# Kernel tuning notes

Measured on AMD Instinct MI355X. Metric: run time of the kernel, lower is better.

The kernel has to match this reference:

```python
import jax, jax.numpy as jnp
import numpy as np

CROP_H, CROP_W = 14, 14
EXTRAP = 0.0


def setup_inputs() -> dict:
    key = jax.random.key(0)
    k1, k2, k3 = jax.random.split(key, 3)
    image = jax.random.normal(k1, (8, 256, 200, 200), dtype=jnp.float32)
    boxes = jax.random.uniform(k2, (512, 4), dtype=jnp.float32)  # normalized [y1,x1,y2,x2]
    box_indices = jax.random.randint(k3, (512,), 0, 8).astype(jnp.int32)
    return {"image": image, "boxes": boxes, "box_indices": box_indices}


def _crop_and_resize(image, boxes, box_indices, crop_h, crop_w, extrap):
    # TF-style crop_and_resize with bilinear sampling (matches crop_and_resize_cpu).
    B, C, H, W = image.shape
    N = boxes.shape[0]
    y1, x1, y2, x2 = boxes[:, 0], boxes[:, 1], boxes[:, 2], boxes[:, 3]
    h_scale = (y2 - y1) * (H - 1) / (crop_h - 1)
    w_scale = (x2 - x1) * (W - 1) / (crop_w - 1)
    in_y = y1[:, None] * (H - 1) + jnp.arange(crop_h, dtype=jnp.float32)[None, :] * h_scale[:, None]  # [N,ch]
    in_x = x1[:, None] * (W - 1) + jnp.arange(crop_w, dtype=jnp.float32)[None, :] * w_scale[:, None]  # [N,cw]
    valid_y = (in_y >= 0) & (in_y <= H - 1)  # [N,ch]
    valid_x = (in_x >= 0) & (in_x <= W - 1)  # [N,cw]

    y_floor = jnp.floor(in_y)
    x_floor = jnp.floor(in_x)
    ly = (in_y - y_floor)[:, :, None, None]  # [N,ch,1,1]
    lx = (in_x - x_floor)[:, None, :, None]  # [N,1,cw,1]
    y0 = jnp.clip(y_floor, 0, H - 1).astype(jnp.int32)
    y1i = jnp.clip(jnp.ceil(in_y), 0, H - 1).astype(jnp.int32)
    x0 = jnp.clip(x_floor, 0, W - 1).astype(jnp.int32)
    x1i = jnp.clip(jnp.ceil(in_x), 0, W - 1).astype(jnp.int32)

    b = box_indices.astype(jnp.int32)[:, None, None]  # [N,1,1]

    def gather(yi, xi):
        # advanced indices [N,ch,cw] separated by ':' slice -> result [N,ch,cw,C]
        return image[b, :, yi[:, :, None], xi[:, None, :]]

    tl = gather(y0, x0)
    tr = gather(y0, x1i)
    bl = gather(y1i, x0)
    br = gather(y1i, x1i)

    top = tl + (tr - tl) * lx
    bot = bl + (br - bl) * lx
    val = top + (bot - top) * ly  # [N,ch,cw,C]

    mask = (valid_y[:, :, None] & valid_x[:, None, :])[:, :, :, None]
    val = jnp.where(mask, val, jnp.float32(extrap))
    return jnp.transpose(val, (0, 3, 1, 2))  # [N,C,ch,cw]


def reference(image, boxes, box_indices):
    return _crop_and_resize(image, boxes, box_indices, CROP_H, CROP_W, EXTRAP)
```

## Files before the change

### kernel.cpp

```cpp
#include <hip/hip_runtime.h>

#define CROP_H 14
#define CROP_W 14
#define NBOX   512
#define CH     256
#define IMH    200
#define IMW    200
#define PER_BOX (CH * CROP_H * CROP_W)
#define BLOCKS_PER_BOX (PER_BOX / 256)

__global__ __launch_bounds__(256) void CropAndResize_60146722013533_kernel(
    const float* __restrict__ image,
    const float* __restrict__ boxes,
    const int*   __restrict__ box_idx,
    float*       __restrict__ out)
{
    const int n = blockIdx.x;
    const int t = threadIdx.x;

    __shared__ int   sy0[CROP_H], sy1[CROP_H], sx0[CROP_W], sx1[CROP_W];
    __shared__ float sly[CROP_H], slx[CROP_W];
    __shared__ int   svy[CROP_H], svx[CROP_W];
    __shared__ int   sb;

    if (t < CROP_H + CROP_W) {
        const float by1 = boxes[n * 4 + 0];
        const float bx1 = boxes[n * 4 + 1];
        const float by2 = boxes[n * 4 + 2];
        const float bx2 = boxes[n * 4 + 3];
        if (t < CROP_H) {
            const int gy = t;
            float h_scale = (by2 - by1) * (float)(IMH - 1) / (float)(CROP_H - 1);
            float in_y = by1 * (float)(IMH - 1) + (float)gy * h_scale;
            svy[gy] = (in_y >= 0.0f && in_y <= (float)(IMH - 1)) ? 1 : 0;
            float yf = floorf(in_y);
            sly[gy] = in_y - yf;
            sy0[gy] = (int)fminf(fmaxf(yf, 0.0f), (float)(IMH - 1));
            sy1[gy] = (int)fminf(fmaxf(ceilf(in_y), 0.0f), (float)(IMH - 1));
        } else {
            const int gx = t - CROP_H;
            float w_scale = (bx2 - bx1) * (float)(IMW - 1) / (float)(CROP_W - 1);
            float in_x = bx1 * (float)(IMW - 1) + (float)gx * w_scale;
            svx[gx] = (in_x >= 0.0f && in_x <= (float)(IMW - 1)) ? 1 : 0;
            float xf = floorf(in_x);
            slx[gx] = in_x - xf;
            sx0[gx] = (int)fminf(fmaxf(xf, 0.0f), (float)(IMW - 1));
            sx1[gx] = (int)fminf(fmaxf(ceilf(in_x), 0.0f), (float)(IMW - 1));
        }
    }
    if (t == 0) sb = box_idx[n];
    __syncthreads();

    const int elem = blockIdx.y * 256 + t;
    const int c  = elem / (CROP_H * CROP_W);
    const int r  = elem - c * (CROP_H * CROP_W);
    const int gy = r / CROP_W;
    const int gx = r - gy * CROP_W;

    const float* base = image + ((size_t)(sb * CH + c)) * (size_t)(IMH * IMW);
    const int y0  = sy0[gy];
    const int y1i = sy1[gy];
    const int x0  = sx0[gx];
    const int x1i = sx1[gx];
    const float ly = sly[gy];
    const float lx = slx[gx];

    const int xb = (x0 < IMW - 2) ? x0 : (IMW - 2);
    const float* rowt = base + y0  * IMW + xb;
    const float* rowb = base + y1i * IMW + xb;
    float2 vt, vb;
    __builtin_memcpy(&vt, rowt, 8);
    __builtin_memcpy(&vb, rowb, 8);

    const float tl = (x0  == xb) ? vt.x : vt.y;
    const float tr = (x1i == xb) ? vt.x : vt.y;
    const float bl = (x0  == xb) ? vb.x : vb.y;
    const float br = (x1i == xb) ? vb.x : vb.y;

    const float top = tl + (tr - tl) * lx;
    const float bot = bl + (br - bl) * lx;
    float val = top + (bot - top) * ly;
    if (!(svy[gy] & svx[gx])) val = 0.0f;

    out[(size_t)n * PER_BOX + elem] = val;
}

extern "C" void kernel_launch(void* const* d_in, const int* in_sizes, int n_in,
                              void* d_out, int out_size, void* d_ws, size_t ws_size,
                              hipStream_t stream) {
    const float* image   = (const float*)d_in[0];
    const float* boxes   = (const float*)d_in[1];
    const int*   box_idx = (const int*)d_in[2];
    float* out = (float*)d_out;

    dim3 grid(NBOX, BLOCKS_PER_BOX, 1);
    dim3 block(256, 1, 1);
    CropAndResize_60146722013533_kernel<<<grid, block, 0, stream>>>(image, boxes, box_idx, out);
}
```

Measured before the change: 493.0 us.

## Map threads to crop positions and loop over channel groups per block

Each block now covers one box and a group of 32 channels. Each thread owns one of the 196 crop positions, computes its sampling coordinates once in registers, and loops over channels, so the shared-memory setup and barrier are gone. Output writes use nontemporal stores. In exchange there are far fewer blocks, 60 of every 256 threads sit idle, and each thread runs a serial loop of dependent loads, which may reduce memory-level parallelism.

After: 530.5 us. +7.6%, slower.

```diff
diff --git a/kernel.cpp b/kernel.cpp
--- a/kernel.cpp
+++ b/kernel.cpp
@@ -6,83 +6,80 @@
 #define CH     256
 #define IMH    200
 #define IMW    200
-#define PER_BOX (CH * CROP_H * CROP_W)
-#define BLOCKS_PER_BOX (PER_BOX / 256)
+#define PLANE   (IMH * IMW)
+#define NPOS    (CROP_H * CROP_W)
+#define PER_BOX (CH * NPOS)
+#define CGROUPS 8
+#define CPG     (CH / CGROUPS)
 
-__global__ __launch_bounds__(256) void CropAndResize_60146722013533_kernel(
+__global__ __launch_bounds__(256, 8) void CropAndResize_60146722013533_kernel(
     const float* __restrict__ image,
     const float* __restrict__ boxes,
     const int*   __restrict__ box_idx,
     float*       __restrict__ out)
 {
-    const int n = blockIdx.x;
-    const int t = threadIdx.x;
+    const int n  = blockIdx.x;
+    const int cg = blockIdx.y;
+    const int t  = threadIdx.x;
+    if (t >= NPOS) return;
 
-    __shared__ int   sy0[CROP_H], sy1[CROP_H], sx0[CROP_W], sx1[CROP_W];
-    __shared__ float sly[CROP_H], slx[CROP_W];
-    __shared__ int   svy[CROP_H], svx[CROP_W];
-    __shared__ int   sb;
+    const int gy = t / CROP_W;
+    const int gx = t - gy * CROP_W;
 
-    if (t < CROP_H + CROP_W) {
-        const float by1 = boxes[n * 4 + 0];
-        const float bx1 = boxes[n * 4 + 1];
-        const float by2 = boxes[n * 4 + 2];
-        const float bx2 = boxes[n * 4 + 3];
-        if (t < CROP_H) {
-            const int gy = t;
-            float h_scale = (by2 - by1) * (float)(IMH - 1) / (float)(CROP_H - 1);
-            float in_y = by1 * (float)(IMH - 1) + (float)gy * h_scale;
-            svy[gy] = (in_y >= 0.0f && in_y <= (float)(IMH - 1)) ? 1 : 0;
-            float yf = floorf(in_y);
-            sly[gy] = in_y - yf;
-            sy0[gy] = (int)fminf(fmaxf(yf, 0.0f), (float)(IMH - 1));
-            sy1[gy] = (int)fminf(fmaxf(ceilf(in_y), 0.0f), (float)(IMH - 1));
-        } else {
-            const int gx = t - CROP_H;
-            float w_scale = (bx2 - bx1) * (float)(IMW - 1) / (float)(CROP_W - 1);
-            float in_x = bx1 * (float)(IMW - 1) + (float)gx * w_scale;
-            svx[gx] = (in_x >= 0.0f && in_x <= (float)(IMW - 1)) ? 1 : 0;
-            float xf = floorf(in_x);
-            slx[gx] = in_x - xf;
-            sx0[gx] = (int)fminf(fmaxf(xf, 0.0f), (float)(IMW - 1));
-            sx1[gx] = (int)fminf(fmaxf(ceilf(in_x), 0.0f), (float)(IMW - 1));
-        }
+    const float by1 = boxes[n * 4 + 0];
+    const float bx1 = boxes[n * 4 + 1];
+    const float by2 = boxes[n * 4 + 2];
+    const float bx2 = boxes[n * 4 + 3];
+    const int   b   = box_idx[n];
+
+    const float h_scale = (by2 - by1) * (float)(IMH - 1) / (float)(CROP_H - 1);
+    const float w_scale = (bx2 - bx1) * (float)(IMW - 1) / (float)(CROP_W - 1);
+    const float in_y = by1 * (float)(IMH - 1) + (float)gy * h_scale;
+    const float in_x = bx1 * (float)(IMW - 1) + (float)gx * w_scale;
+
+    const bool valid = (in_y >= 0.0f) && (in_y <= (float)(IMH - 1)) &&
+                       (in_x >= 0.0f) && (in_x <= (float)(IMW - 1));
+
+    const float yf = floorf(in_y);
+    const float xf = floorf(in_x);
+    const float ly = in_y - yf;
+    const float lx = in_x - xf;
+
+    const int y0  = (int)fminf(fmaxf(yf,          0.0f), (float)(IMH - 1));
+    const int y1i = (int)fminf(fmaxf(ceilf(in_y), 0.0f), (float)(IMH - 1));
+    const int x0  = (int)fminf(fmaxf(xf,          0.0f), (float)(IMW - 1));
+    const int x1i = (int)fminf(fmaxf(ceilf(in_x), 0.0f), (float)(IMW - 1));
+
+    const int  xb    = (x0 < IMW - 2) ? x0 : (IMW - 2);
+    const int  offt  = y0  * IMW + xb;
+    const int  offb  = y1i * IMW + xb;
+    const bool selt0 = (x0  == xb);
+    const bool selt1 = (x1i == xb);
+
+    const float* plane = image + (size_t)(b * CH + cg * CPG) * (size_t)PLANE;
+    float*       o     = out + (size_t)n * PER_BOX + (size_t)(cg * CPG) * NPOS + t;
+
+    #pragma unroll 4
+    for (int c = 0; c < CPG; ++c) {
+        float2 vt, vb;
+        __builtin_memcpy(&vt, plane + offt, 8);
+        __builtin_memcpy(&vb, plane + offb, 8);
+
+        const float tl = selt0 ? vt.x : vt.y;
+        const float tr = selt1 ? vt.x : vt.y;
+        const float bl = selt0 ? vb.x : vb.y;
+        const float br = selt1 ? vb.x : vb.y;
+
+        const float top = tl + (tr - tl) * lx;
+        const float bot = bl + (br - bl) * lx;
+        float val = top + (bot - top) * ly;
+        if (!valid) val = 0.0f;
+
+        __builtin_nontemporal_store(val, o);
+
+        plane += PLANE;
+        o     += NPOS;
     }
-    if (t == 0) sb = box_idx[n];
-    __syncthreads();
-
-    const int elem = blockIdx.y * 256 + t;
-    const int c  = elem / (CROP_H * CROP_W);
-    const int r  = elem - c * (CROP_H * CROP_W);
-    const int gy = r / CROP_W;
-    const int gx = r - gy * CROP_W;
-
-    const float* base = image + ((size_t)(sb * CH + c)) * (size_t)(IMH * IMW);
-    const int y0  = sy0[gy];
-    const int y1i = sy1[gy];
-    const int x0  = sx0[gx];
-    const int x1i = sx1[gx];
-    const float ly = sly[gy];
-    const float lx = slx[gx];
-
-    const int xb = (x0 < IMW - 2) ? x0 : (IMW - 2);
-    const float* rowt = base + y0  * IMW + xb;
-    const float* rowb = base + y1i * IMW + xb;
-    float2 vt, vb;
-    __builtin_memcpy(&vt, rowt, 8);
-    __builtin_memcpy(&vb, rowb, 8);
-
-    const float tl = (x0  == xb) ? vt.x : vt.y;
-    const float tr = (x1i == xb) ? vt.x : vt.y;
-    const float bl = (x0  == xb) ? vb.x : vb.y;
-    const float br = (x1i == xb) ? vb.x : vb.y;
-
-    const float top = tl + (tr - tl) * lx;
-    const float bot = bl + (br - bl) * lx;
-    float val = top + (bot - top) * ly;
-    if (!(svy[gy] & svx[gx])) val = 0.0f;
-
-    out[(size_t)n * PER_BOX + elem] = val;
 }
 
 extern "C" void kernel_launch(void* const* d_in, const int* in_sizes, int n_in,
@@ -93,7 +90,7 @@
     const int*   box_idx = (const int*)d_in[2];
     float* out = (float*)d_out;
 
-    dim3 grid(NBOX, BLOCKS_PER_BOX, 1);
+    dim3 grid(NBOX, CGROUPS, 1);
     dim3 block(256, 1, 1);
     CropAndResize_60146722013533_kernel<<<grid, block, 0, stream>>>(image, boxes, box_idx, out);
 }
```

## Stage needed image rows in LDS per channel and loop channels per block

Applied to the files above, without the earlier changes.

Each block now handles one box and a group of 32 channels, cooperatively loading the two source rows per crop row into shared memory with coalesced float4 loads, then bilinearly sampling from LDS. This replaces scattered per-output float2 gathers from global memory. It reads full image rows (more bytes than needed) and adds two block barriers per channel, and it uses nontemporal output stores.

New measurement: 667.5 us. 35.4% more time.

```diff
diff --git a/kernel.cpp b/kernel.cpp
--- a/kernel.cpp
+++ b/kernel.cpp
@@ -6,21 +6,29 @@
 #define CH     256
 #define IMH    200
 #define IMW    200
-#define PER_BOX (CH * CROP_H * CROP_W)
-#define BLOCKS_PER_BOX (PER_BOX / 256)
+#define PLANE   (IMH * IMW)
+#define NPOS    (CROP_H * CROP_W)
+#define PER_BOX (CH * NPOS)
+#define CGROUPS 8
+#define CPG     (CH / CGROUPS)
+#define NROWS   (2 * CROP_H)
+#define F4_PER_CH (CROP_H * 2 * (IMW / 4))
 
-__global__ __launch_bounds__(256) void CropAndResize_60146722013533_kernel(
+__global__ __launch_bounds__(256, 7) void CropAndResize_60146722013533_kernel(
     const float* __restrict__ image,
     const float* __restrict__ boxes,
     const int*   __restrict__ box_idx,
     float*       __restrict__ out)
 {
-    const int n = blockIdx.x;
-    const int t = threadIdx.x;
+    const int n  = blockIdx.x;
+    const int cg = blockIdx.y;
+    const int t  = threadIdx.x;
 
-    __shared__ int   sy0[CROP_H], sy1[CROP_H], sx0[CROP_W], sx1[CROP_W];
+    __shared__ float slds[NROWS][IMW];
+    __shared__ int   sy0[CROP_H], sy1r[CROP_H];
     __shared__ float sly[CROP_H], slx[CROP_W];
     __shared__ int   svy[CROP_H], svx[CROP_W];
+    __shared__ int   sx0[CROP_W], sx1[CROP_W];
     __shared__ int   sb;
 
     if (t < CROP_H + CROP_W) {
@@ -35,8 +43,9 @@
             svy[gy] = (in_y >= 0.0f && in_y <= (float)(IMH - 1)) ? 1 : 0;
             float yf = floorf(in_y);
             sly[gy] = in_y - yf;
-            sy0[gy] = (int)fminf(fmaxf(yf, 0.0f), (float)(IMH - 1));
-            sy1[gy] = (int)fminf(fmaxf(ceilf(in_y), 0.0f), (float)(IMH - 1));
+            int y0 = (int)fminf(fmaxf(yf, 0.0f), (float)(IMH - 1));
+            sy0[gy]  = y0;
+            sy1r[gy] = (y0 < IMH - 1) ? (y0 + 1) : (IMH - 1);
         } else {
             const int gx = t - CROP_H;
             float w_scale = (bx2 - bx1) * (float)(IMW - 1) / (float)(CROP_W - 1);
@@ -51,38 +60,52 @@
     if (t == 0) sb = box_idx[n];
     __syncthreads();
 
-    const int elem = blockIdx.y * 256 + t;
-    const int c  = elem / (CROP_H * CROP_W);
-    const int r  = elem - c * (CROP_H * CROP_W);
-    const int gy = r / CROP_W;
-    const int gx = r - gy * CROP_W;
+    const int gy = t / CROP_W;
+    const int gx = t - gy * CROP_W;
+    int   x0 = 0, x1i = 0, vmask = 0, rowt = 0;
+    float ly = 0.0f, lx = 0.0f;
+    if (t < NPOS) {
+        x0    = sx0[gx];
+        x1i   = sx1[gx];
+        ly    = sly[gy];
+        lx    = slx[gx];
+        vmask = svy[gy] & svx[gx];
+        rowt  = 2 * gy;
+    }
 
-    const float* base = image + ((size_t)(sb * CH + c)) * (size_t)(IMH * IMW);
-    const int y0  = sy0[gy];
-    const int y1i = sy1[gy];
-    const int x0  = sx0[gx];
-    const int x1i = sx1[gx];
-    const float ly = sly[gy];
-    const float lx = slx[gx];
+    const float* pb = image + (size_t)(sb * CH + cg * CPG) * (size_t)PLANE;
+    float*       o  = out + (size_t)n * PER_BOX + (size_t)(cg * CPG) * NPOS + t;
 
-    const int xb = (x0 < IMW - 2) ? x0 : (IMW - 2);
-    const float* rowt = base + y0  * IMW + xb;
-    const float* rowb = base + y1i * IMW + xb;
-    float2 vt, vb;
-    __builtin_memcpy(&vt, rowt, 8);
-    __builtin_memcpy(&vb, rowb, 8);
+    for (int c = 0; c < CPG; ++c) {
+        #pragma unroll
+        for (int k = t; k < F4_PER_CH; k += 256) {
+            const int gyr  = k / 100;
+            const int w    = k - gyr * 100;
+            const int half = (w >= 50) ? 1 : 0;
+            const int wq   = w - half * 50;
+            const int row  = half ? sy1r[gyr] : sy0[gyr];
+            float4 v;
+            __builtin_memcpy(&v, pb + (size_t)row * IMW + wq * 4, 16);
+            *(float4*)&slds[gyr * 2 + half][wq * 4] = v;
+        }
+        __syncthreads();
 
-    const float tl = (x0  == xb) ? vt.x : vt.y;
-    const float tr = (x1i == xb) ? vt.x : vt.y;
-    const float bl = (x0  == xb) ? vb.x : vb.y;
-    const float br = (x1i == xb) ? vb.x : vb.y;
+        if (t < NPOS) {
+            const float tl = slds[rowt    ][x0];
+            const float tr = slds[rowt    ][x1i];
+            const float bl = slds[rowt + 1][x0];
+            const float br = slds[rowt + 1][x1i];
+            const float top = tl + (tr - tl) * lx;
+            const float bot = bl + (br - bl) * lx;
+            float val = top + (bot - top) * ly;
+            if (!vmask) val = 0.0f;
+            __builtin_nontemporal_store(val, o);
+        }
+        __syncthreads();
 
-    const float top = tl + (tr - tl) * lx;
-    const float bot = bl + (br - bl) * lx;
-    float val = top + (bot - top) * ly;
-    if (!(svy[gy] & svx[gx])) val = 0.0f;
-
-    out[(size_t)n * PER_BOX + elem] = val;
+        pb += PLANE;
+        o  += NPOS;
+    }
 }
 
 extern "C" void kernel_launch(void* const* d_in, const int* in_sizes, int n_in,
@@ -93,7 +116,7 @@
     const int*   box_idx = (const int*)d_in[2];
     float* out = (float*)d_out;
 
-    dim3 grid(NBOX, BLOCKS_PER_BOX, 1);
+    dim3 grid(NBOX, CGROUPS, 1);
     dim3 block(256, 1, 1);
     CropAndResize_60146722013533_kernel<<<grid, block, 0, stream>>>(image, boxes, box_idx, out);
 }
```

## Stage needed image rows in LDS per box-channel with float4 loads

Applied to the files above, without the earlier changes.

Switches to one block per (box, channel). The block cooperatively loads the 28 needed source rows, restricted to the box's x-span, into shared memory with float4 loads, then 196 threads interpolate from LDS and write with nontemporal stores. The aim is coalesced, vectorized global reads in place of scattered float2 gathers. In exchange, 60 of 256 threads sit idle during compute, there is an extra barrier, and the launch-bounds occupancy hint is raised. Loads can over-fetch when boxes are wide, and the final float4 may read past the row end for x near the right edge.

New measurement: 746.6 us. 1.51x slower.

```diff
diff --git a/kernel.cpp b/kernel.cpp
--- a/kernel.cpp
+++ b/kernel.cpp
@@ -6,18 +6,23 @@
 #define CH     256
 #define IMH    200
 #define IMW    200
-#define PER_BOX (CH * CROP_H * CROP_W)
-#define BLOCKS_PER_BOX (PER_BOX / 256)
+#define PLANE   (IMH * IMW)
+#define NPOS    (CROP_H * CROP_W)
+#define PER_BOX (CH * NPOS)
+#define NROWS   (2 * CROP_H)
+#define LDS_STRIDE 204
 
-__global__ __launch_bounds__(256) void CropAndResize_60146722013533_kernel(
+__global__ __launch_bounds__(256, 7) void CropAndResize_60146722013533_kernel(
     const float* __restrict__ image,
     const float* __restrict__ boxes,
     const int*   __restrict__ box_idx,
     float*       __restrict__ out)
 {
     const int n = blockIdx.x;
+    const int c = blockIdx.y;
     const int t = threadIdx.x;
 
+    __shared__ float slds[NROWS][LDS_STRIDE];
     __shared__ int   sy0[CROP_H], sy1[CROP_H], sx0[CROP_W], sx1[CROP_W];
     __shared__ float sly[CROP_H], slx[CROP_W];
     __shared__ int   svy[CROP_H], svx[CROP_W];
@@ -51,38 +56,56 @@
     if (t == 0) sb = box_idx[n];
     __syncthreads();
 
-    const int elem = blockIdx.y * 256 + t;
-    const int c  = elem / (CROP_H * CROP_W);
-    const int r  = elem - c * (CROP_H * CROP_W);
-    const int gy = r / CROP_W;
-    const int gx = r - gy * CROP_W;
+    int xlo = sx0[0], xhi = sx1[0];
+    #pragma unroll
+    for (int i = 1; i < CROP_W; ++i) {
+        xlo = min(xlo, sx0[i]);
+        xhi = max(xhi, sx1[i]);
+    }
+    const int f4lo  = xlo >> 2;
+    const int nf4   = (xhi >> 2) - f4lo + 1;
+    const int xbase = f4lo << 2;
 
-    const float* base = image + ((size_t)(sb * CH + c)) * (size_t)(IMH * IMW);
-    const int y0  = sy0[gy];
-    const int y1i = sy1[gy];
-    const int x0  = sx0[gx];
-    const int x1i = sx1[gx];
-    const float ly = sly[gy];
-    const float lx = slx[gx];
+    const float* __restrict__ pb =
+        image + (size_t)(sb * CH + c) * (size_t)PLANE;
 
-    const int xb = (x0 < IMW - 2) ? x0 : (IMW - 2);
-    const float* rowt = base + y0  * IMW + xb;
-    const float* rowb = base + y1i * IMW + xb;
-    float2 vt, vb;
-    __builtin_memcpy(&vt, rowt, 8);
-    __builtin_memcpy(&vb, rowb, 8);
+    {
+        const int f4 = t & 63;
+        const int w0 = t >> 6;
+        if (f4 < nf4) {
+            const float* src = pb + xbase + f4 * 4;
+            #pragma unroll
+            for (int rr = w0; rr < NROWS; rr += 4) {
+                const int gyr = rr >> 1;
+                const int row = (rr & 1) ? sy1[gyr] : sy0[gyr];
+                float4 v;
+                __builtin_memcpy(&v, src + row * IMW, 16);
+                *(float4*)&slds[rr][f4 * 4] = v;
+            }
+        }
+    }
+    __syncthreads();
 
-    const float tl = (x0  == xb) ? vt.x : vt.y;
-    const float tr = (x1i == xb) ? vt.x : vt.y;
-    const float bl = (x0  == xb) ? vb.x : vb.y;
-    const float br = (x1i == xb) ? vb.x : vb.y;
+    if (t < NPOS) {
+        const int gy = t / CROP_W;
+        const int gx = t - gy * CROP_W;
+        const int x0  = sx0[gx] - xbase;
+        const int x1i = sx1[gx] - xbase;
+        const float ly = sly[gy];
+        const float lx = slx[gx];
 
-    const float top = tl + (tr - tl) * lx;
-    const float bot = bl + (br - bl) * lx;
-    float val = top + (bot - top) * ly;
-    if (!(svy[gy] & svx[gx])) val = 0.0f;
+        const float tl = slds[2 * gy    ][x0];
+        const float tr = slds[2 * gy    ][x1i];
+        const float bl = slds[2 * gy + 1][x0];
+        const float br = slds[2 * gy + 1][x1i];
 
-    out[(size_t)n * PER_BOX + elem] = val;
+        const float top = tl + (tr - tl) * lx;
+        const float bot = bl + (br - bl) * lx;
+        float val = top + (bot - top) * ly;
+        if (!(svy[gy] & svx[gx])) val = 0.0f;
+
+        __builtin_nontemporal_store(val, out + (size_t)n * PER_BOX + c * NPOS + t);
+    }
 }
 
 extern "C" void kernel_launch(void* const* d_in, const int* in_sizes, int n_in,
@@ -93,7 +116,7 @@
     const int*   box_idx = (const int*)d_in[2];
     float* out = (float*)d_out;
 
-    dim3 grid(NBOX, BLOCKS_PER_BOX, 1);
+    dim3 grid(NBOX, CH, 1);
     dim3 block(256, 1, 1);
     CropAndResize_60146722013533_kernel<<<grid, block, 0, stream>>>(image, boxes, box_idx, out);
 }
```
